# Optimization experiments

Hardware: AMD Instinct MI355X
Metric: run time of the kernel (lower is better)

## Reference

```python
import jax, jax.numpy as jnp
import numpy as np

HID = 2048
TAU_MIN, TAU_MAX, DT, SPARSITY = 1.0, 20.0, 0.5, 0.15
LN_EPS = 1e-5


def setup_inputs() -> dict:
    key = jax.random.key(0)
    ks = jax.random.split(key, 6)
    B, S, H = 16, 512, HID
    x = jax.random.normal(ks[0], (B, S, H), jnp.float32)
    # input_projection: Linear(H, H) (kaiming-uniform-ish scale)
    Wi = jax.random.normal(ks[1], (H, H), jnp.float32) * (1.0 / np.sqrt(H))
    b = jnp.zeros((H,), jnp.float32)
    # recurrent weights, xavier_normal gain=2.0, then sparsified by fixed mask
    Wr = jax.random.normal(ks[2], (H, H), jnp.float32) * (2.0 * np.sqrt(2.0 / (H + H)))
    mask = (jax.random.uniform(ks[3], (H, H)) < SPARSITY).astype(jnp.float32)
    Wr = Wr * mask
    # tau ~ exp(U(log tau_min, log tau_max))
    log_tau = jax.random.uniform(ks[4], (H,)) * (np.log(TAU_MAX) - np.log(TAU_MIN)) + np.log(TAU_MIN)
    tau = jnp.exp(log_tau).astype(jnp.float32)
    gamma = jnp.ones((H,), jnp.float32)
    beta = jnp.zeros((H,), jnp.float32)
    return {"x": x, "Wi": Wi, "b": b, "Wr": Wr, "mask": mask, "tau": tau, "gamma": gamma, "beta": beta}


def reference(x, Wi, b, Wr, mask, tau, gamma, beta):
    # x: [B, S, H]
    B, S, H = x.shape
    # input projection for all timesteps at once (math-equivalent to per-step Linear)
    inp = jnp.einsum('bsh,oh->bso', x, Wi) + b  # [B, S, H]
    Wm = Wr * mask                              # masked recurrent weights [H, H]
    tau_c = jnp.clip(tau, TAU_MIN, TAU_MAX)
    alpha = jnp.clip(DT / tau_c, 0.0, 1.0)      # [H]

    def step(state, inp_t):
        # state: [B, H], inp_t: [B, H]
        target = jnp.tanh(inp_t + state @ Wm.T)
        state = jnp.clip(state + alpha * (target - state), -1.0, 1.0)
        return state, state

    state0 = jnp.zeros((B, H), x.dtype)
    _, outs = jax.lax.scan(step, state0, jnp.swapaxes(inp, 0, 1))  # [S, B, H]
    outs = jnp.swapaxes(outs, 0, 1)  # [B, S, H]
    # LayerNorm over last dim (biased variance, as torch)
    mu = outs.mean(-1, keepdims=True)
    var = ((outs - mu) ** 2).mean(-1, keepdims=True)
    return (outs - mu) * jax.lax.rsqrt(var + LN_EPS) * gamma + beta
```

## Files before the change

### kernel.cpp

```cpp
#include <hip/hip_runtime.h>
#include <math.h>

typedef __bf16 bf16_t;
typedef __bf16 bf16x8 __attribute__((ext_vector_type(8)));
typedef float f32x4 __attribute__((ext_vector_type(4)));
typedef int i32x4 __attribute__((ext_vector_type(4)));
typedef unsigned int u32;

#define HID 2048
#define NBATCH 16
#define SEQLEN 512
#define MTOT (NBATCH * SEQLEN)
#define NBLK 32
#define RTHREADS 512
#define LN_EPS 1e-5f

__global__ __launch_bounds__(256) void gemm_proj(
    const float* __restrict__ X,
    const float* __restrict__ Wi,
    const float* __restrict__ bias,
    float* __restrict__ C,
    int* __restrict__ flags)
{
    __shared__ bf16_t lA[128 * 32];
    __shared__ bf16_t lB[128 * 32];
    const int tid = threadIdx.x;
    if (blockIdx.x == 0 && blockIdx.y == 0) {
        if (tid < NBLK) flags[tid] = 0;
    }
    const int lane = tid & 63;
    const int wv = tid >> 6;
    const int bn = blockIdx.x * 128;
    const int bm = blockIdx.y * 128;
    const int wr = (wv >> 1) * 64;
    const int wc = (wv & 1) * 64;

    f32x4 zero = {0.f, 0.f, 0.f, 0.f};
    f32x4 acc[4][4];
#pragma unroll
    for (int i = 0; i < 4; ++i)
#pragma unroll
        for (int j = 0; j < 4; ++j) acc[i][j] = zero;

    for (int k0 = 0; k0 < HID; k0 += 32) {
        __syncthreads();
#pragma unroll
        for (int c = 0; c < 2; ++c) {
            const int chunk = c * 256 + tid;
            const int row = chunk >> 2;
            const int kp = (chunk & 3) ^ (row & 3);
            {
                const float* s = X + (size_t)(bm + row) * HID + k0 + kp * 8;
                float4 a0 = *(const float4*)s;
                float4 a1 = *(const float4*)(s + 4);
                bf16x8 v;
                v[0] = (bf16_t)a0.x; v[1] = (bf16_t)a0.y; v[2] = (bf16_t)a0.z; v[3] = (bf16_t)a0.w;
                v[4] = (bf16_t)a1.x; v[5] = (bf16_t)a1.y; v[6] = (bf16_t)a1.z; v[7] = (bf16_t)a1.w;
                *(bf16x8*)(lA + chunk * 8) = v;
            }
            {
                const float* s = Wi + (size_t)(bn + row) * HID + k0 + kp * 8;
                float4 a0 = *(const float4*)s;
                float4 a1 = *(const float4*)(s + 4);
                bf16x8 v;
                v[0] = (bf16_t)a0.x; v[1] = (bf16_t)a0.y; v[2] = (bf16_t)a0.z; v[3] = (bf16_t)a0.w;
                v[4] = (bf16_t)a1.x; v[5] = (bf16_t)a1.y; v[6] = (bf16_t)a1.z; v[7] = (bf16_t)a1.w;
                *(bf16x8*)(lB + chunk * 8) = v;
            }
        }
        __syncthreads();

        bf16x8 af[4], bfr[4];
#pragma unroll
        for (int i = 0; i < 4; ++i) {
            const int row = wr + i * 16 + (lane & 15);
            const int ck = (lane >> 4) ^ (row & 3);
            af[i] = *(const bf16x8*)(lA + row * 32 + ck * 8);
        }
#pragma unroll
        for (int j = 0; j < 4; ++j) {
            const int row = wc + j * 16 + (lane & 15);
            const int ck = (lane >> 4) ^ (row & 3);
            bfr[j] = *(const bf16x8*)(lB + row * 32 + ck * 8);
        }
#pragma unroll
        for (int i = 0; i < 4; ++i)
#pragma unroll
            for (int j = 0; j < 4; ++j)
                acc[i][j] = __builtin_amdgcn_mfma_f32_16x16x32_bf16(af[i], bfr[j], acc[i][j], 0, 0, 0);
    }

#pragma unroll
    for (int j = 0; j < 4; ++j) {
        const int col = bn + wc + j * 16 + (lane & 15);
        const float bv = bias[col];
#pragma unroll
        for (int i = 0; i < 4; ++i) {
#pragma unroll
            for (int r = 0; r < 4; ++r) {
                const int row = bm + wr + i * 16 + (lane >> 4) * 4 + r;
                C[(size_t)row * HID + col] = acc[i][j][r] + bv;
            }
        }
    }
}

__global__ __launch_bounds__(RTHREADS, 1) void recurrent(
    const float* __restrict__ Wr,
    const float* __restrict__ mask,
    const float* __restrict__ tau,
    float* __restrict__ io,
    bf16_t* __restrict__ st0,
    bf16_t* __restrict__ st1,
    int* __restrict__ flags)
{
    const int tid = threadIdx.x;
    const int lane = tid & 63;
    const int wv = tid >> 6;
    const int colbase = blockIdx.x * 64;

    __shared__ float red[8][16][68];

    bf16x8 wf[32];
    {
        const int kb = wv * 256 + (lane >> 4) * 8;
#pragma unroll
        for (int ct = 0; ct < 4; ++ct) {
            const int gc = colbase + ct * 16 + (lane & 15);
#pragma unroll
            for (int kf = 0; kf < 8; ++kf) {
                const size_t off = (size_t)gc * HID + kb + kf * 32;
                float4 a0 = *(const float4*)(Wr + off);
                float4 a1 = *(const float4*)(Wr + off + 4);
                float4 m0 = *(const float4*)(mask + off);
                float4 m1 = *(const float4*)(mask + off + 4);
                bf16x8 v;
                v[0] = (bf16_t)(a0.x * m0.x); v[1] = (bf16_t)(a0.y * m0.y);
                v[2] = (bf16_t)(a0.z * m0.z); v[3] = (bf16_t)(a0.w * m0.w);
                v[4] = (bf16_t)(a1.x * m1.x); v[5] = (bf16_t)(a1.y * m1.y);
                v[6] = (bf16_t)(a1.z * m1.z); v[7] = (bf16_t)(a1.w * m1.w);
                wf[ct * 8 + kf] = v;
            }
        }
    }

    const int row = tid >> 5;
    const int uc  = (tid & 31) * 2;
    const int gcol = colbase + uc;
    float al0, al1;
    {
        float tv0 = fminf(fmaxf(tau[gcol],     1.0f), 20.0f);
        float tv1 = fminf(fmaxf(tau[gcol + 1], 1.0f), 20.0f);
        al0 = fminf(fmaxf(0.5f / tv0, 0.0f), 1.0f);
        al1 = fminf(fmaxf(0.5f / tv1, 0.0f), 1.0f);
    }

    float s_old0 = 0.f, s_old1 = 0.f;
    float2 cin = *(const float2*)(io + (size_t)row * (SEQLEN * HID) + gcol);

    const int akb = wv * 256 + (lane >> 4) * 8;
    bf16_t* cur = st0;
    bf16_t* nxt = st1;

    {
        float z0 = fminf(fmaxf(cin.x, -15.f), 15.f);
        float z1 = fminf(fmaxf(cin.y, -15.f), 15.f);
        const float e0 = __expf(2.0f * z0), e1 = __expf(2.0f * z1);
        float sn0 = fminf(fmaxf(al0 * ((e0 - 1.0f) / (e0 + 1.0f)), -1.0f), 1.0f);
        float sn1 = fminf(fmaxf(al1 * ((e1 - 1.0f) / (e1 + 1.0f)), -1.0f), 1.0f);
        union { bf16_t b[2]; u32 u; } p;
        p.b[0] = (bf16_t)sn0; p.b[1] = (bf16_t)sn1;
        __hip_atomic_store((u32*)(nxt + (size_t)row * HID + gcol), p.u,
                           __ATOMIC_RELAXED, __HIP_MEMORY_SCOPE_AGENT);
        float2 ov; ov.x = sn0; ov.y = sn1;
        *(float2*)(io + (size_t)row * (SEQLEN * HID) + gcol) = ov;
        s_old0 = sn0; s_old1 = sn1;
        cin = *(const float2*)(io + (size_t)row * (SEQLEN * HID) + HID + gcol);
        __syncthreads();
        if (tid == 0)
            __hip_atomic_store(flags + (int)blockIdx.x, 1,
                               __ATOMIC_RELAXED, __HIP_MEMORY_SCOPE_AGENT);
        bf16_t* tmp = cur; cur = nxt; nxt = tmp;
    }

    for (int t = 1; t < SEQLEN; ++t) {
        if (wv == 0) {
            int v;
            do {
                v = __hip_atomic_load(flags + (lane & 31),
                                      __ATOMIC_RELAXED, __HIP_MEMORY_SCOPE_AGENT);
            } while (__ballot(v < t) != 0ull);
        }
        __builtin_amdgcn_sched_barrier(0);
        asm volatile("s_barrier" ::: "memory");
        __builtin_amdgcn_sched_barrier(0);

        const bf16_t* ab = cur + (size_t)(lane & 15) * HID + akb;
        union uf { i32x4 i; bf16x8 v; } a0_, a1_, a2_, a3_, a4_, a5_, a6_, a7_;
        asm volatile("global_load_dwordx4 %0, %1, off sc0 sc1"            : "=v"(a0_.i) : "v"(ab) : "memory");
        asm volatile("global_load_dwordx4 %0, %1, off offset:64 sc0 sc1"  : "=v"(a1_.i) : "v"(ab) : "memory");
        asm volatile("global_load_dwordx4 %0, %1, off offset:128 sc0 sc1" : "=v"(a2_.i) : "v"(ab) : "memory");
        asm volatile("global_load_dwordx4 %0, %1, off offset:192 sc0 sc1" : "=v"(a3_.i) : "v"(ab) : "memory");
        asm volatile("global_load_dwordx4 %0, %1, off offset:256 sc0 sc1" : "=v"(a4_.i) : "v"(ab) : "memory");
        asm volatile("global_load_dwordx4 %0, %1, off offset:320 sc0 sc1" : "=v"(a5_.i) : "v"(ab) : "memory");
        asm volatile("global_load_dwordx4 %0, %1, off offset:384 sc0 sc1" : "=v"(a6_.i) : "v"(ab) : "memory");
        asm volatile("global_load_dwordx4 %0, %1, off offset:448 sc0 sc1" : "=v"(a7_.i) : "v"(ab) : "memory");
        const int tn = (t < SEQLEN - 1) ? (t + 1) : t;
        float2 cin_next = *(const float2*)(io + (size_t)row * (SEQLEN * HID) + (size_t)tn * HID + gcol);

        f32x4 acc0 = {0.f,0.f,0.f,0.f}, acc1 = {0.f,0.f,0.f,0.f};
        f32x4 acc2 = {0.f,0.f,0.f,0.f}, acc3 = {0.f,0.f,0.f,0.f};

        asm volatile("s_waitcnt vmcnt(5)" ::: "memory");
        __builtin_amdgcn_sched_barrier(0);
#define MF(u_, kf) \
        acc0 = __builtin_amdgcn_mfma_f32_16x16x32_bf16(u_.v, wf[kf],      acc0, 0, 0, 0); \
        acc1 = __builtin_amdgcn_mfma_f32_16x16x32_bf16(u_.v, wf[8 + kf],  acc1, 0, 0, 0); \
        acc2 = __builtin_amdgcn_mfma_f32_16x16x32_bf16(u_.v, wf[16 + kf], acc2, 0, 0, 0); \
        acc3 = __builtin_amdgcn_mfma_f32_16x16x32_bf16(u_.v, wf[24 + kf], acc3, 0, 0, 0);
        MF(a0_, 0) MF(a1_, 1) MF(a2_, 2) MF(a3_, 3)
        asm volatile("s_waitcnt vmcnt(1)" ::: "memory");
        __builtin_amdgcn_sched_barrier(0);
        MF(a4_, 4) MF(a5_, 5) MF(a6_, 6) MF(a7_, 7)
#undef MF

        {
            const int r0 = (lane >> 4) * 4;
            const int cA = lane & 15;
#pragma unroll
            for (int r = 0; r < 4; ++r) {
                red[wv][r0 + r][cA]      = acc0[r];
                red[wv][r0 + r][16 + cA] = acc1[r];
                red[wv][r0 + r][32 + cA] = acc2[r];
                red[wv][r0 + r][48 + cA] = acc3[r];
            }
        }
        asm volatile("s_waitcnt lgkmcnt(0)" ::: "memory");
        __builtin_amdgcn_sched_barrier(0);
        asm volatile("s_barrier" ::: "memory");
        __builtin_amdgcn_sched_barrier(0);

        float rec0 = 0.f, rec1 = 0.f;
#pragma unroll
        for (int q = 0; q < 8; ++q) {
            float2 s = *(const float2*)&red[q][row][uc];
            rec0 += s.x; rec1 += s.y;
        }

        float z0 = fminf(fmaxf(cin.x + rec0, -15.f), 15.f);
        float z1 = fminf(fmaxf(cin.y + rec1, -15.f), 15.f);
        const float e0 = __expf(2.0f * z0), e1 = __expf(2.0f * z1);
        const float tg0 = (e0 - 1.0f) / (e0 + 1.0f);
        const float tg1 = (e1 - 1.0f) / (e1 + 1.0f);
        float sn0 = fminf(fmaxf(s_old0 + al0 * (tg0 - s_old0), -1.0f), 1.0f);
        float sn1 = fminf(fmaxf(s_old1 + al1 * (tg1 - s_old1), -1.0f), 1.0f);

        union { bf16_t b[2]; u32 u; } p;
        p.b[0] = (bf16_t)sn0; p.b[1] = (bf16_t)sn1;
        __hip_atomic_store((u32*)(nxt + (size_t)row * HID + gcol), p.u,
                           __ATOMIC_RELAXED, __HIP_MEMORY_SCOPE_AGENT);
        float2 ov; ov.x = sn0; ov.y = sn1;
        *(float2*)(io + (size_t)row * (SEQLEN * HID) + (size_t)t * HID + gcol) = ov;

        asm volatile("s_waitcnt vmcnt(0)" ::: "memory");
        __builtin_amdgcn_sched_barrier(0);
        asm volatile("s_barrier" ::: "memory");
        __builtin_amdgcn_sched_barrier(0);
        if (t != SEQLEN - 1 && tid == 0)
            __hip_atomic_store(flags + (int)blockIdx.x, t + 1,
                               __ATOMIC_RELAXED, __HIP_MEMORY_SCOPE_AGENT);

        s_old0 = sn0; s_old1 = sn1;
        cin = cin_next;
        bf16_t* tmp = cur; cur = nxt; nxt = tmp;
    }
}

__global__ __launch_bounds__(256) void ln_kernel(
    float* __restrict__ io,
    const float* __restrict__ gamma,
    const float* __restrict__ beta)
{
    const size_t row = blockIdx.x;
    float* p = io + row * HID;
    const int tid = threadIdx.x;
    float4 v0 = *(const float4*)(p + tid * 4);
    float4 v1 = *(const float4*)(p + 1024 + tid * 4);
    float s  = v0.x + v0.y + v0.z + v0.w + v1.x + v1.y + v1.z + v1.w;
    float ss = v0.x * v0.x + v0.y * v0.y + v0.z * v0.z + v0.w * v0.w
             + v1.x * v1.x + v1.y * v1.y + v1.z * v1.z + v1.w * v1.w;
#pragma unroll
    for (int off = 32; off > 0; off >>= 1) {
        s  += __shfl_down(s, off, 64);
        ss += __shfl_down(ss, off, 64);
    }
    __shared__ float rs[4], rss[4];
    if ((tid & 63) == 0) { rs[tid >> 6] = s; rss[tid >> 6] = ss; }
    __syncthreads();
    s  = rs[0] + rs[1] + rs[2] + rs[3];
    ss = rss[0] + rss[1] + rss[2] + rss[3];
    const float mu = s * (1.f / HID);
    const float var = ss * (1.f / HID) - mu * mu;
    const float inv = rsqrtf(var + LN_EPS);
    const int c0 = tid * 4, c1 = 1024 + tid * 4;
    float4 g0 = *(const float4*)(gamma + c0);
    float4 g1 = *(const float4*)(gamma + c1);
    float4 b0 = *(const float4*)(beta + c0);
    float4 b1 = *(const float4*)(beta + c1);
    float4 o0, o1;
    o0.x = (v0.x - mu) * inv * g0.x + b0.x;
    o0.y = (v0.y - mu) * inv * g0.y + b0.y;
    o0.z = (v0.z - mu) * inv * g0.z + b0.z;
    o0.w = (v0.w - mu) * inv * g0.w + b0.w;
    o1.x = (v1.x - mu) * inv * g1.x + b1.x;
    o1.y = (v1.y - mu) * inv * g1.y + b1.y;
    o1.z = (v1.z - mu) * inv * g1.z + b1.z;
    o1.w = (v1.w - mu) * inv * g1.w + b1.w;
    *(float4*)(p + tid * 4) = o0;
    *(float4*)(p + 1024 + tid * 4) = o1;
}

extern "C" void kernel_launch(void* const* d_in, const int* in_sizes, int n_in,
                              void* d_out, int out_size, void* d_ws, size_t ws_size,
                              hipStream_t stream)
{
    const float* x     = (const float*)d_in[0];
    const float* Wi    = (const float*)d_in[1];
    const float* bias  = (const float*)d_in[2];
    const float* Wr    = (const float*)d_in[3];
    const float* mask  = (const float*)d_in[4];
    const float* tau   = (const float*)d_in[5];
    const float* gamma = (const float*)d_in[6];
    const float* beta  = (const float*)d_in[7];
    float* out = (float*)d_out;

    bf16_t* st0 = (bf16_t*)d_ws;
    bf16_t* st1 = st0 + (size_t)NBATCH * HID;
    int* flags  = (int*)(st1 + (size_t)NBATCH * HID);

    gemm_proj<<<dim3(16, 64), 256, 0, stream>>>(x, Wi, bias, out, flags);
    recurrent<<<NBLK, RTHREADS, 0, stream>>>(Wr, mask, tau, out, st0, st1, flags);
    ln_kernel<<<MTOT, 256, 0, stream>>>(out, gamma, beta);
}
```

Baseline: 2.346 ms.

## Split batch into two independent halves interleaved to hide grid sync latency

The recurrent kernel now treats the 16-row batch as two independent 8-row chains, A and B. Each chain has its own double-buffered bf16 state and its own set of per-block progress flags, and each time step runs an A phase and then a B phase. The aim is that while one half waits on the cross-block flags, the other half's work keeps the pipeline busy, so part of the global synchronisation latency is hidden. The cost is twice as many barriers and MFMA passes per time step, and the MFMAs still use 16-row tiles with only 8 valid rows, so half of that work is wasted.

```diff
diff --git a/kernel.cpp b/kernel.cpp
--- a/kernel.cpp
+++ b/kernel.cpp
@@ -14,6 +14,7 @@
 #define NBLK 32
 #define RTHREADS 512
 #define LN_EPS 1e-5f
+#define CHB 8
 
 __global__ __launch_bounds__(256) void gemm_proj(
     const float* __restrict__ X,
@@ -26,7 +27,7 @@
     __shared__ bf16_t lB[128 * 32];
     const int tid = threadIdx.x;
     if (blockIdx.x == 0 && blockIdx.y == 0) {
-        if (tid < NBLK) flags[tid] = 0;
+        if (tid < 128) flags[tid] = 0;
     }
     const int lane = tid & 63;
     const int wv = tid >> 6;
@@ -110,8 +111,10 @@
     const float* __restrict__ mask,
     const float* __restrict__ tau,
     float* __restrict__ io,
-    bf16_t* __restrict__ st0,
-    bf16_t* __restrict__ st1,
+    bf16_t* __restrict__ stA0,
+    bf16_t* __restrict__ stA1,
+    bf16_t* __restrict__ stB0,
+    bf16_t* __restrict__ stB1,
     int* __restrict__ flags)
 {
     const int tid = threadIdx.x;
@@ -119,7 +122,7 @@
     const int wv = tid >> 6;
     const int colbase = blockIdx.x * 64;
 
-    __shared__ float red[8][16][68];
+    __shared__ float red[8][8][68];
 
     bf16x8 wf[32];
     {
@@ -144,46 +147,65 @@
         }
     }
 
-    const int row = tid >> 5;
-    const int uc  = (tid & 31) * 2;
-    const int gcol = colbase + uc;
-    float al0, al1;
+    const int urow = wv;
+    const int ucol = lane;
+    const int gcol = colbase + ucol;
+    const size_t SH = (size_t)SEQLEN * HID;
+    float al;
     {
-        float tv0 = fminf(fmaxf(tau[gcol],     1.0f), 20.0f);
-        float tv1 = fminf(fmaxf(tau[gcol + 1], 1.0f), 20.0f);
-        al0 = fminf(fmaxf(0.5f / tv0, 0.0f), 1.0f);
-        al1 = fminf(fmaxf(0.5f / tv1, 0.0f), 1.0f);
-    }
-
-    float s_old0 = 0.f, s_old1 = 0.f;
-    float2 cin = *(const float2*)(io + (size_t)row * (SEQLEN * HID) + gcol);
+        float tv = fminf(fmaxf(tau[gcol], 1.0f), 20.0f);
+        al = fminf(fmaxf(0.5f / tv, 0.0f), 1.0f);
+    }
+
+    float s_oldA = 0.f, s_oldB = 0.f;
+    float cinA = io[(size_t)urow * SH + gcol];
+    float cinB = io[(size_t)(CHB + urow) * SH + gcol];
 
     const int akb = wv * 256 + (lane >> 4) * 8;
-    bf16_t* cur = st0;
-    bf16_t* nxt = st1;
+    bf16_t *curA = stA1, *nxtA = stA0;
+    bf16_t *curB = stB1, *nxtB = stB0;
 
     {
-        float z0 = fminf(fmaxf(cin.x, -15.f), 15.f);
-        float z1 = fminf(fmaxf(cin.y, -15.f), 15.f);
-        const float e0 = __expf(2.0f * z0), e1 = __expf(2.0f * z1);
-        float sn0 = fminf(fmaxf(al0 * ((e0 - 1.0f) / (e0 + 1.0f)), -1.0f), 1.0f);
-        float sn1 = fminf(fmaxf(al1 * ((e1 - 1.0f) / (e1 + 1.0f)), -1.0f), 1.0f);
-        union { bf16_t b[2]; u32 u; } p;
-        p.b[0] = (bf16_t)sn0; p.b[1] = (bf16_t)sn1;
-        __hip_atomic_store((u32*)(nxt + (size_t)row * HID + gcol), p.u,
-                           __ATOMIC_RELAXED, __HIP_MEMORY_SCOPE_AGENT);
-        float2 ov; ov.x = sn0; ov.y = sn1;
-        *(float2*)(io + (size_t)row * (SEQLEN * HID) + gcol) = ov;
-        s_old0 = sn0; s_old1 = sn1;
-        cin = *(const float2*)(io + (size_t)row * (SEQLEN * HID) + HID + gcol);
+        float zA = fminf(fmaxf(cinA, -15.f), 15.f);
+        float zB = fminf(fmaxf(cinB, -15.f), 15.f);
+        const float eA = __expf(2.0f * zA), eB = __expf(2.0f * zB);
+        float snA = fminf(fmaxf(al * ((eA - 1.0f) / (eA + 1.0f)), -1.0f), 1.0f);
+        float snB = fminf(fmaxf(al * ((eB - 1.0f) / (eB + 1.0f)), -1.0f), 1.0f);
+        float pA = __shfl_xor(snA, 1);
+        float pB = __shfl_xor(snB, 1);
+        if ((lane & 1) == 0) {
+            union { bf16_t b[2]; u32 u; } q;
+            q.b[0] = (bf16_t)snA; q.b[1] = (bf16_t)pA;
+            __hip_atomic_store((u32*)(curA + (size_t)urow * HID + gcol), q.u,
+                               __ATOMIC_RELAXED, __HIP_MEMORY_SCOPE_AGENT);
+            q.b[0] = (bf16_t)snB; q.b[1] = (bf16_t)pB;
+            __hip_atomic_store((u32*)(curB + (size_t)urow * HID + gcol), q.u,
+                               __ATOMIC_RELAXED, __HIP_MEMORY_SCOPE_AGENT);
+        }
+        io[(size_t)urow * SH + gcol] = snA;
+        io[(size_t)(CHB + urow) * SH + gcol] = snB;
+        s_oldA = snA; s_oldB = snB;
+        cinA = io[(size_t)urow * SH + HID + gcol];
+        cinB = io[(size_t)(CHB + urow) * SH + HID + gcol];
         __syncthreads();
-        if (tid == 0)
+        if (tid == 0) {
             __hip_atomic_store(flags + (int)blockIdx.x, 1,
                                __ATOMIC_RELAXED, __HIP_MEMORY_SCOPE_AGENT);
-        bf16_t* tmp = cur; cur = nxt; nxt = tmp;
-    }
+            __hip_atomic_store(flags + 64 + (int)blockIdx.x, 1,
+                               __ATOMIC_RELAXED, __HIP_MEMORY_SCOPE_AGENT);
+        }
+    }
+
+#define SB __builtin_amdgcn_sched_barrier(0)
+#define MF(u_, kf) \
+        acc0 = __builtin_amdgcn_mfma_f32_16x16x32_bf16(u_.v, wf[kf],      acc0, 0, 0, 0); \
+        acc1 = __builtin_amdgcn_mfma_f32_16x16x32_bf16(u_.v, wf[8 + kf],  acc1, 0, 0, 0); \
+        acc2 = __builtin_amdgcn_mfma_f32_16x16x32_bf16(u_.v, wf[16 + kf], acc2, 0, 0, 0); \
+        acc3 = __builtin_amdgcn_mfma_f32_16x16x32_bf16(u_.v, wf[24 + kf], acc3, 0, 0, 0);
 
     for (int t = 1; t < SEQLEN; ++t) {
+        const int tn = (t < SEQLEN - 1) ? (t + 1) : t;
+
         if (wv == 0) {
             int v;
             do {
@@ -191,89 +213,137 @@
                                       __ATOMIC_RELAXED, __HIP_MEMORY_SCOPE_AGENT);
             } while (__ballot(v < t) != 0ull);
         }
-        __builtin_amdgcn_sched_barrier(0);
-        asm volatile("s_barrier" ::: "memory");
-        __builtin_amdgcn_sched_barrier(0);
-
-        const bf16_t* ab = cur + (size_t)(lane & 15) * HID + akb;
-        union uf { i32x4 i; bf16x8 v; } a0_, a1_, a2_, a3_, a4_, a5_, a6_, a7_;
-        asm volatile("global_load_dwordx4 %0, %1, off sc0 sc1"            : "=v"(a0_.i) : "v"(ab) : "memory");
-        asm volatile("global_load_dwordx4 %0, %1, off offset:64 sc0 sc1"  : "=v"(a1_.i) : "v"(ab) : "memory");
-        asm volatile("global_load_dwordx4 %0, %1, off offset:128 sc0 sc1" : "=v"(a2_.i) : "v"(ab) : "memory");
-        asm volatile("global_load_dwordx4 %0, %1, off offset:192 sc0 sc1" : "=v"(a3_.i) : "v"(ab) : "memory");
-        asm volatile("global_load_dwordx4 %0, %1, off offset:256 sc0 sc1" : "=v"(a4_.i) : "v"(ab) : "memory");
-        asm volatile("global_load_dwordx4 %0, %1, off offset:320 sc0 sc1" : "=v"(a5_.i) : "v"(ab) : "memory");
-        asm volatile("global_load_dwordx4 %0, %1, off offset:384 sc0 sc1" : "=v"(a6_.i) : "v"(ab) : "memory");
-        asm volatile("global_load_dwordx4 %0, %1, off offset:448 sc0 sc1" : "=v"(a7_.i) : "v"(ab) : "memory");
-        const int tn = (t < SEQLEN - 1) ? (t + 1) : t;
-        float2 cin_next = *(const float2*)(io + (size_t)row * (SEQLEN * HID) + (size_t)tn * HID + gcol);
-
-        f32x4 acc0 = {0.f,0.f,0.f,0.f}, acc1 = {0.f,0.f,0.f,0.f};
-        f32x4 acc2 = {0.f,0.f,0.f,0.f}, acc3 = {0.f,0.f,0.f,0.f};
-
-        asm volatile("s_waitcnt vmcnt(5)" ::: "memory");
-        __builtin_amdgcn_sched_barrier(0);
-#define MF(u_, kf) \
-        acc0 = __builtin_amdgcn_mfma_f32_16x16x32_bf16(u_.v, wf[kf],      acc0, 0, 0, 0); \
-        acc1 = __builtin_amdgcn_mfma_f32_16x16x32_bf16(u_.v, wf[8 + kf],  acc1, 0, 0, 0); \
-        acc2 = __builtin_amdgcn_mfma_f32_16x16x32_bf16(u_.v, wf[16 + kf], acc2, 0, 0, 0); \
-        acc3 = __builtin_amdgcn_mfma_f32_16x16x32_bf16(u_.v, wf[24 + kf], acc3, 0, 0, 0);
-        MF(a0_, 0) MF(a1_, 1) MF(a2_, 2) MF(a3_, 3)
-        asm volatile("s_waitcnt vmcnt(1)" ::: "memory");
-        __builtin_amdgcn_sched_barrier(0);
-        MF(a4_, 4) MF(a5_, 5) MF(a6_, 6) MF(a7_, 7)
+        SB; asm volatile("s_barrier" ::: "memory"); SB;
+        {
+            const bf16_t* ab = curA + (size_t)(lane & 7) * HID + akb;
+            union uf { i32x4 i; bf16x8 v; } a0_, a1_, a2_, a3_, a4_, a5_, a6_, a7_;
+            asm volatile("global_load_dwordx4 %0, %1, off sc0 sc1"            : "=v"(a0_.i) : "v"(ab) : "memory");
+            asm volatile("global_load_dwordx4 %0, %1, off offset:64 sc0 sc1"  : "=v"(a1_.i) : "v"(ab) : "memory");
+            asm volatile("global_load_dwordx4 %0, %1, off offset:128 sc0 sc1" : "=v"(a2_.i) : "v"(ab) : "memory");
+            asm volatile("global_load_dwordx4 %0, %1, off offset:192 sc0 sc1" : "=v"(a3_.i) : "v"(ab) : "memory");
+            asm volatile("global_load_dwordx4 %0, %1, off offset:256 sc0 sc1" : "=v"(a4_.i) : "v"(ab) : "memory");
+            asm volatile("global_load_dwordx4 %0, %1, off offset:320 sc0 sc1" : "=v"(a5_.i) : "v"(ab) : "memory");
+            asm volatile("global_load_dwordx4 %0, %1, off offset:384 sc0 sc1" : "=v"(a6_.i) : "v"(ab) : "memory");
+            asm volatile("global_load_dwordx4 %0, %1, off offset:448 sc0 sc1" : "=v"(a7_.i) : "v"(ab) : "memory");
+            float cinN = io[(size_t)urow * SH + (size_t)tn * HID + gcol];
+
+            f32x4 acc0 = {0.f,0.f,0.f,0.f}, acc1 = {0.f,0.f,0.f,0.f};
+            f32x4 acc2 = {0.f,0.f,0.f,0.f}, acc3 = {0.f,0.f,0.f,0.f};
+            asm volatile("s_waitcnt vmcnt(5)" ::: "memory"); SB;
+            MF(a0_, 0) MF(a1_, 1) MF(a2_, 2) MF(a3_, 3)
+            asm volatile("s_waitcnt vmcnt(1)" ::: "memory"); SB;
+            MF(a4_, 4) MF(a5_, 5) MF(a6_, 6) MF(a7_, 7)
+
+            if (lane < 32) {
+                const int r0 = (lane >> 4) * 4;
+                const int cA = lane & 15;
+#pragma unroll
+                for (int r = 0; r < 4; ++r) {
+                    red[wv][r0 + r][cA]      = acc0[r];
+                    red[wv][r0 + r][16 + cA] = acc1[r];
+                    red[wv][r0 + r][32 + cA] = acc2[r];
+                    red[wv][r0 + r][48 + cA] = acc3[r];
+                }
+            }
+            asm volatile("s_waitcnt lgkmcnt(0)" ::: "memory"); SB;
+            asm volatile("s_barrier" ::: "memory"); SB;
+
+            float rec = 0.f;
+#pragma unroll
+            for (int q = 0; q < 8; ++q) rec += red[q][urow][ucol];
+
+            float z = fminf(fmaxf(cinA + rec, -15.f), 15.f);
+            const float e = __expf(2.0f * z);
+            const float tg = (e - 1.0f) / (e + 1.0f);
+            float sn = fminf(fmaxf(s_oldA + al * (tg - s_oldA), -1.0f), 1.0f);
+
+            float pp = __shfl_xor(sn, 1);
+            if ((lane & 1) == 0) {
+                union { bf16_t b[2]; u32 u; } q;
+                q.b[0] = (bf16_t)sn; q.b[1] = (bf16_t)pp;
+                __hip_atomic_store((u32*)(nxtA + (size_t)urow * HID + gcol), q.u,
+                                   __ATOMIC_RELAXED, __HIP_MEMORY_SCOPE_AGENT);
+            }
+            asm volatile("s_waitcnt vmcnt(0)" ::: "memory"); SB;
+            asm volatile("s_barrier" ::: "memory"); SB;
+            if (t != SEQLEN - 1 && tid == 0)
+                __hip_atomic_store(flags + (int)blockIdx.x, t + 1,
+                                   __ATOMIC_RELAXED, __HIP_MEMORY_SCOPE_AGENT);
+            io[(size_t)urow * SH + (size_t)t * HID + gcol] = sn;
+            s_oldA = sn; cinA = cinN;
+            bf16_t* tmp = curA; curA = nxtA; nxtA = tmp;
+        }
+
+        if (wv == 0) {
+            int v;
+            do {
+                v = __hip_atomic_load(flags + 64 + (lane & 31),
+                                      __ATOMIC_RELAXED, __HIP_MEMORY_SCOPE_AGENT);
+            } while (__ballot(v < t) != 0ull);
+        }
+        SB; asm volatile("s_barrier" ::: "memory"); SB;
+        {
+            const bf16_t* ab = curB + (size_t)(lane & 7) * HID + akb;
+            union uf { i32x4 i; bf16x8 v; } a0_, a1_, a2_, a3_, a4_, a5_, a6_, a7_;
+            asm volatile("global_load_dwordx4 %0, %1, off sc0 sc1"            : "=v"(a0_.i) : "v"(ab) : "memory");
+            asm volatile("global_load_dwordx4 %0, %1, off offset:64 sc0 sc1"  : "=v"(a1_.i) : "v"(ab) : "memory");
+            asm volatile("global_load_dwordx4 %0, %1, off offset:128 sc0 sc1" : "=v"(a2_.i) : "v"(ab) : "memory");
+            asm volatile("global_load_dwordx4 %0, %1, off offset:192 sc0 sc1" : "=v"(a3_.i) : "v"(ab) : "memory");
+            asm volatile("global_load_dwordx4 %0, %1, off offset:256 sc0 sc1" : "=v"(a4_.i) : "v"(ab) : "memory");
+            asm volatile("global_load_dwordx4 %0, %1, off offset:320 sc0 sc1" : "=v"(a5_.i) : "v"(ab) : "memory");
+            asm volatile("global_load_dwordx4 %0, %1, off offset:384 sc0 sc1" : "=v"(a6_.i) : "v"(ab) : "memory");
+            asm volatile("global_load_dwordx4 %0, %1, off offset:448 sc0 sc1" : "=v"(a7_.i) : "v"(ab) : "memory");
+            float cinN = io[(size_t)(CHB + urow) * SH + (size_t)tn * HID + gcol];
+
+            f32x4 acc0 = {0.f,0.f,0.f,0.f}, acc1 = {0.f,0.f,0.f,0.f};
+            f32x4 acc2 = {0.f,0.f,0.f,0.f}, acc3 = {0.f,0.f,0.f,0.f};
+            asm volatile("s_waitcnt vmcnt(5)" ::: "memory"); SB;
+            MF(a0_, 0) MF(a1_, 1) MF(a2_, 2) MF(a3_, 3)
+            asm volatile("s_waitcnt vmcnt(1)" ::: "memory"); SB;
+            MF(a4_, 4) MF(a5_, 5) MF(a6_, 6) MF(a7_, 7)
+
+            if (lane < 32) {
+                const int r0 = (lane >> 4) * 4;
+                const int cA = lane & 15;
+#pragma unroll
+                for (int r = 0; r < 4; ++r) {
+                    red[wv][r0 + r][cA]      = acc0[r];
+                    red[wv][r0 + r][16 + cA] = acc1[r];
+                    red[wv][r0 + r][32 + cA] = acc2[r];
+                    red[wv][r0 + r][48 + cA] = acc3[r];
+                }
+            }
+            asm volatile("s_waitcnt lgkmcnt(0)" ::: "memory"); SB;
+            asm volatile("s_barrier" ::: "memory"); SB;
+
+            float rec = 0.f;
+#pragma unroll
+            for (int q = 0; q < 8; ++q) rec += red[q][urow][ucol];
+
+            float z = fminf(fmaxf(cinB + rec, -15.f), 15.f);
+            const float e = __expf(2.0f * z);
+            const float tg = (e - 1.0f) / (e + 1.0f);
+            float sn = fminf(fmaxf(s_oldB + al * (tg - s_oldB), -1.0f), 1.0f);
+
+            float pp = __shfl_xor(sn, 1);
+            if ((lane & 1) == 0) {
+                union { bf16_t b[2]; u32 u; } q;
+                q.b[0] = (bf16_t)sn; q.b[1] = (bf16_t)pp;
+                __hip_atomic_store((u32*)(nxtB + (size_t)urow * HID + gcol), q.u,
+                                   __ATOMIC_RELAXED, __HIP_MEMORY_SCOPE_AGENT);
+            }
+            asm volatile("s_waitcnt vmcnt(0)" ::: "memory"); SB;
+            asm volatile("s_barrier" ::: "memory"); SB;
+            if (t != SEQLEN - 1 && tid == 0)
+                __hip_atomic_store(flags + 64 + (int)blockIdx.x, t + 1,
+                                   __ATOMIC_RELAXED, __HIP_MEMORY_SCOPE_AGENT);
+            io[(size_t)(CHB + urow) * SH + (size_t)t * HID + gcol] = sn;
+            s_oldB = sn; cinB = cinN;
+            bf16_t* tmp = curB; curB = nxtB; nxtB = tmp;
+        }
+    }
 #undef MF
-
-        {
-            const int r0 = (lane >> 4) * 4;
-            const int cA = lane & 15;
-#pragma unroll
-            for (int r = 0; r < 4; ++r) {
-                red[wv][r0 + r][cA]      = acc0[r];
-                red[wv][r0 + r][16 + cA] = acc1[r];
-                red[wv][r0 + r][32 + cA] = acc2[r];
-                red[wv][r0 + r][48 + cA] = acc3[r];
-            }
-        }
-        asm volatile("s_waitcnt lgkmcnt(0)" ::: "memory");
-        __builtin_amdgcn_sched_barrier(0);
-        asm volatile("s_barrier" ::: "memory");
-        __builtin_amdgcn_sched_barrier(0);
-
-        float rec0 = 0.f, rec1 = 0.f;
-#pragma unroll
-        for (int q = 0; q < 8; ++q) {
-            float2 s = *(const float2*)&red[q][row][uc];
-            rec0 += s.x; rec1 += s.y;
-        }
-
-        float z0 = fminf(fmaxf(cin.x + rec0, -15.f), 15.f);
-        float z1 = fminf(fmaxf(cin.y + rec1, -15.f), 15.f);
-        const float e0 = __expf(2.0f * z0), e1 = __expf(2.0f * z1);
-        const float tg0 = (e0 - 1.0f) / (e0 + 1.0f);
-        const float tg1 = (e1 - 1.0f) / (e1 + 1.0f);
-        float sn0 = fminf(fmaxf(s_old0 + al0 * (tg0 - s_old0), -1.0f), 1.0f);
-        float sn1 = fminf(fmaxf(s_old1 + al1 * (tg1 - s_old1), -1.0f), 1.0f);
-
-        union { bf16_t b[2]; u32 u; } p;
-        p.b[0] = (bf16_t)sn0; p.b[1] = (bf16_t)sn1;
-        __hip_atomic_store((u32*)(nxt + (size_t)row * HID + gcol), p.u,
-                           __ATOMIC_RELAXED, __HIP_MEMORY_SCOPE_AGENT);
-        float2 ov; ov.x = sn0; ov.y = sn1;
-        *(float2*)(io + (size_t)row * (SEQLEN * HID) + (size_t)t * HID + gcol) = ov;
-
-        asm volatile("s_waitcnt vmcnt(0)" ::: "memory");
-        __builtin_amdgcn_sched_barrier(0);
-        asm volatile("s_barrier" ::: "memory");
-        __builtin_amdgcn_sched_barrier(0);
-        if (t != SEQLEN - 1 && tid == 0)
-            __hip_atomic_store(flags + (int)blockIdx.x, t + 1,
-                               __ATOMIC_RELAXED, __HIP_MEMORY_SCOPE_AGENT);
-
-        s_old0 = sn0; s_old1 = sn1;
-        cin = cin_next;
-        bf16_t* tmp = cur; cur = nxt; nxt = tmp;
-    }
+#undef SB
 }
 
 __global__ __launch_bounds__(256) void ln_kernel(
@@ -334,11 +404,14 @@
     const float* beta  = (const float*)d_in[7];
     float* out = (float*)d_out;
 
-    bf16_t* st0 = (bf16_t*)d_ws;
-    bf16_t* st1 = st0 + (size_t)NBATCH * HID;
-    int* flags  = (int*)(st1 + (size_t)NBATCH * HID);
+    bf16_t* stA0 = (bf16_t*)d_ws;
+    bf16_t* stA1 = stA0 + (size_t)CHB * HID;
+    bf16_t* stB0 = stA1 + (size_t)CHB * HID;
+    bf16_t* stB1 = stB0 + (size_t)CHB * HID;
+    int* flags   = (int*)(stB1 + (size_t)CHB * HID);
 
     gemm_proj<<<dim3(16, 64), 256, 0, stream>>>(x, Wi, bias, out, flags);
-    recurrent<<<NBLK, RTHREADS, 0, stream>>>(Wr, mask, tau, out, st0, st1, flags);
+    recurrent<<<NBLK, RTHREADS, 0, stream>>>(Wr, mask, tau, out,
+                                             stA0, stA1, stB0, stB1, flags);
     ln_kernel<<<MTOT, 256, 0, stream>>>(out, gamma, beta);
 }
```

After: 3.918 ms. 1.67x slower.
